# Optimization experiments

Hardware: AMD Instinct MI355X
Metric: run time of the kernel (lower is better)

## Reference

```python
import jax, jax.numpy as jnp
import numpy as np

H = 2048      # hidden_dim
DI = 4096     # intermediate_size
N = 128       # state_size
NH = 64       # num_heads
P = 64        # head_dim
K = 4         # conv kernel
CH = 256      # chunk size
L = 4096      # seq len
DT_MIN, DT_MAX = 1e-3, 1e2


def setup_inputs() -> dict:
    key = jax.random.key(0)
    ks = jax.random.split(key, 8)
    conv_dim = DI + 2 * N
    x = jax.random.normal(ks[0], (L, H), jnp.float32)
    W_in = jax.random.normal(ks[1], (DI + 2 * N + NH, H), jnp.float32) / np.sqrt(H)
    conv_w = jax.random.normal(ks[2], (conv_dim, 1, K), jnp.float32) / np.sqrt(K)
    conv_b = jax.random.normal(ks[3], (conv_dim,), jnp.float32) * 0.01
    u = jax.random.uniform(ks[4], (NH,))
    dt = jnp.exp(u * (np.log(0.1) - np.log(0.001)) + np.log(0.001))
    dt = jnp.maximum(dt, 1e-4)
    dt_bias = dt + jnp.log(-jnp.expm1(-dt))   # inverse-softplus init
    A_log = jnp.log(jax.random.uniform(ks[5], (NH,), minval=1.0, maxval=16.0))
    D = jnp.ones((NH,), jnp.float32)
    norm_w = jnp.ones((DI,), jnp.float32)
    W_out = jax.random.normal(ks[6], (H, DI), jnp.float32) / np.sqrt(DI)
    return dict(x=x, W_in=W_in, conv_w=conv_w, conv_b=conv_b, dt_bias=dt_bias,
                A_log=A_log, D=D, norm_w=norm_w, W_out=W_out)


def _causal_decay(a):
    # a: [..., T] per-step log-decays -> exp(segment sum) as lower-tri [..., T, T]
    T = a.shape[-1]
    strict = jnp.tril(jnp.ones((T, T), bool), -1)
    full = jnp.tril(jnp.ones((T, T), bool), 0)
    s = jnp.cumsum(jnp.where(strict, a[..., None], 0.0), axis=-2)
    return jnp.where(full, jnp.exp(s), 0.0)


def reference(x, W_in, conv_w, conv_b, dt_bias, A_log, D, norm_w, W_out):
    conv_dim = DI + 2 * N
    xBCdt = x @ W_in.T                                  # [L, DI+2N+NH]
    xBC, dt = xBCdt[:, :conv_dim], xBCdt[:, conv_dim:]
    # causal depthwise conv1d + SiLU
    z = jax.lax.conv_general_dilated(
        xBC.T[None], conv_w, (1,), [(K - 1, 0)],
        dimension_numbers=('NCH', 'OIH', 'NCH'),
        feature_group_count=conv_dim)[0] + conv_b[:, None]
    xBC = jax.nn.silu(z.T)                              # [L, conv_dim]
    x_ssm = xBC[:, :DI].reshape(L, NH, P)
    Bm = xBC[:, DI:DI + N]                              # [L, N] shared over heads
    Cm = xBC[:, DI + N:]                                # [L, N]
    dt = jnp.clip(jax.nn.softplus(dt + dt_bias), DT_MIN, DT_MAX)  # [L, NH]
    A = -jnp.exp(A_log.astype(jnp.float32))             # [NH]
    dA = dt * A                                         # [L, NH]
    xdt = x_ssm * dt[:, :, None]                        # [L, NH, P]
    nc = L // CH
    xc = xdt.reshape(nc, CH, NH, P)
    Bc = Bm.reshape(nc, CH, N)
    Cc = Cm.reshape(nc, CH, N)
    dAc = dA.reshape(nc, CH, NH)
    A_cs = jnp.cumsum(dAc, axis=1)                      # [c, k, h]
    # intra-chunk (diagonal blocks)
    Lmat = _causal_decay(dAc.transpose(0, 2, 1))        # [c, h, k, k]
    Y_diag = jnp.einsum('ckn,csn,chks,cshp->ckhp', Cc, Bc, Lmat, xc)
    # per-chunk right states
    decay_states = jnp.exp(A_cs[:, -1:, :] - A_cs)      # [c, k, h]
    states = jnp.einsum('ckn,ckh,ckhp->chpn', Bc, decay_states, xc)
    # inter-chunk recurrence (no initial state)
    chunk_sum = A_cs[:, -1, :].T                        # [h, c]
    dec = _causal_decay(jnp.pad(chunk_sum, ((0, 0), (1, 0))))  # [h, c+1, c+1]
    states = jnp.concatenate([jnp.zeros((1, NH, P, N), states.dtype), states], 0)
    new_states = jnp.einsum('hzc,chpn->zhpn', dec, states)      # [c+1, h, p, n]
    prev = new_states[:-1]                              # [c, h, p, n]
    Y_off = jnp.einsum('ckn,chpn,ckh->ckhp', Cc, prev, jnp.exp(A_cs))
    Y = (Y_diag + Y_off).reshape(L, NH, P) + x_ssm * D[None, :, None]
    y = Y.reshape(L, DI)
    # RMSNorm
    var = jnp.mean(jnp.square(y.astype(jnp.float32)), -1, keepdims=True)
    y = (y * jax.lax.rsqrt(var + 1e-6)) * norm_w
    return y @ W_out.T
```

## Files before the change

### kernel.cpp

```cpp
#include <hip/hip_runtime.h>


typedef __bf16 bf16;
typedef __bf16 bf16x8 __attribute__((ext_vector_type(8)));
typedef __bf16 bf16x4 __attribute__((ext_vector_type(4)));
typedef float  f32x4  __attribute__((ext_vector_type(4)));

#define DEV static __device__ __forceinline__

DEV f32x4 mfma16(bf16x8 a, bf16x8 b, f32x4 c) {
  return __builtin_amdgcn_mfma_f32_16x16x32_bf16(a, b, c, 0, 0, 0);
}

DEV void gll16(const bf16* g, bf16* l) {
  __builtin_amdgcn_global_load_lds(
      (const __attribute__((address_space(1))) unsigned int*)g,
      (__attribute__((address_space(3))) unsigned int*)l, 16, 0, 0);
}

#define BAR()   asm volatile("s_barrier" ::: "memory")
#define VMW(n)  asm volatile("s_waitcnt vmcnt(" #n ")" ::: "memory")

template <int NT, int LD, bool DTC>
__global__ __launch_bounds__(512, 4) void gemm_kernel(
    const bf16* __restrict__ Abase, const bf16* __restrict__ Bbase,
    bf16* __restrict__ C0, bf16* __restrict__ C1, float* __restrict__ dtf,
    int ldc, int ntN) {
  __shared__ __align__(16) bf16 lds[3 * 12288];
  const int tid = threadIdx.x;
  const int wid = tid >> 6, lane = tid & 63;
  const int lrow = lane & 15;
  const int lc = lane >> 4;
  const int wm = wid & 3, wn = wid >> 2;
  const int bx = blockIdx.x / ntN, by = blockIdx.x % ntN;
  const int row0 = bx * 256, col0 = by * 128;
  const bf16* A = Abase + (size_t)blockIdx.y * (NT * 32);
  const bf16* B = Bbase + (size_t)blockIdx.y * (NT * 32);

  const bf16* gA[2];
  const bf16* gB0;
#pragma unroll
  for (int q = 0; q < 2; ++q) {
    int P = q * 8192 + tid * 16;
    int Lq = P ^ (((P >> 7) & 3) << 4);
    int srow = Lq >> 6;
    int selem = (Lq & 63) >> 1;
    gA[q] = A + (size_t)(row0 + srow) * LD + selem;
  }
  {
    int P = tid * 16;
    int Lq = P ^ (((P >> 7) & 3) << 4);
    int srow = Lq >> 6;
    int selem = (Lq & 63) >> 1;
    gB0 = B + (size_t)(col0 + srow) * LD + selem;
  }
  auto stage = [&](int s, int ko) {
    bf16* sl = lds + s * 12288;
    gll16(gA[0] + ko, sl + tid * 8);
    gll16(gA[1] + ko, sl + 4096 + tid * 8);
    gll16(gB0 + ko, sl + 8192 + tid * 8);
  };
  auto rdA = [&](int s, int m) -> bf16x8 {
    int row = wm * 64 + m * 16 + lrow;
    int off = row * 64 + ((lc ^ ((row >> 1) & 3)) << 4);
    return *(const bf16x8*)((const char*)lds + s * 24576 + off);
  };
  auto rdB = [&](int s, int n) -> bf16x8 {
    int row = wn * 64 + n * 16 + lrow;
    int off = row * 64 + ((lc ^ ((row >> 1) & 3)) << 4);
    return *(const bf16x8*)((const char*)lds + s * 24576 + 16384 + off);
  };

  f32x4 acc[4][4] = {};
  stage(0, 0);
  stage(1, 32);
  int rs = 0, ws = 2;
  for (int t = 0; t < NT; ++t) {
    if (t + 1 < NT) { VMW(3); } else { VMW(0); }
    BAR();
    if (t + 2 < NT) stage(ws, (t + 2) * 32);
    bf16x8 b0 = rdB(rs, 0), b1 = rdB(rs, 1), b2 = rdB(rs, 2), b3 = rdB(rs, 3);
#pragma unroll
    for (int m = 0; m < 4; ++m) {
      bf16x8 a = rdA(rs, m);
      acc[m][0] = mfma16(a, b0, acc[m][0]);
      acc[m][1] = mfma16(a, b1, acc[m][1]);
      acc[m][2] = mfma16(a, b2, acc[m][2]);
      acc[m][3] = mfma16(a, b3, acc[m][3]);
    }
    rs = (rs == 2) ? 0 : rs + 1;
    ws = (ws == 2) ? 0 : ws + 1;
  }
  bf16* C = blockIdx.y ? C1 : C0;
  const int orow = lc * 4;
#pragma unroll
  for (int m = 0; m < 4; ++m)
#pragma unroll
    for (int n = 0; n < 4; ++n)
#pragma unroll
      for (int i = 0; i < 4; ++i) {
        int r = row0 + wm * 64 + m * 16 + orow + i;
        int c = col0 + wn * 64 + n * 16 + lrow;
        C[(size_t)r * ldc + c] = (bf16)acc[m][n][i];
      }
  if (DTC && by == 34 && wn == 0) {
#pragma unroll
    for (int m = 0; m < 4; ++m)
#pragma unroll
      for (int n = 0; n < 4; ++n)
#pragma unroll
        for (int i = 0; i < 4; ++i) {
          int r = row0 + wm * 64 + m * 16 + orow + i;
          int h = n * 16 + lrow;
          dtf[(size_t)r * 64 + h] = acc[m][n][i];
        }
  }
}

__global__ __launch_bounds__(256) void add2b_kernel(
    const bf16* __restrict__ a, const bf16* __restrict__ b,
    float* __restrict__ o, long n8) {
  long i = (long)blockIdx.x * blockDim.x + threadIdx.x;
  long stride = (long)gridDim.x * blockDim.x;
  for (; i < n8; i += stride) {
    bf16x8 va = ((const bf16x8*)a)[i];
    bf16x8 vb = ((const bf16x8*)b)[i];
    float4 o0, o1;
    o0.x = (float)va[0] + (float)vb[0];
    o0.y = (float)va[1] + (float)vb[1];
    o0.z = (float)va[2] + (float)vb[2];
    o0.w = (float)va[3] + (float)vb[3];
    o1.x = (float)va[4] + (float)vb[4];
    o1.y = (float)va[5] + (float)vb[5];
    o1.z = (float)va[6] + (float)vb[6];
    o1.w = (float)va[7] + (float)vb[7];
    ((float4*)o)[i * 2] = o0;
    ((float4*)o)[i * 2 + 1] = o1;
  }
}

__global__ __launch_bounds__(256) void cast_all_kernel(
    const float* __restrict__ x, bf16* __restrict__ xb,
    const float* __restrict__ W_in, bf16* __restrict__ winb,
    const float* __restrict__ W_out, bf16* __restrict__ woutb) {
  const long stride = (long)gridDim.x * blockDim.x;
  const long base = (long)blockIdx.x * blockDim.x + threadIdx.x;
  const long nx = (long)4096 * 2048 / 4;
  for (long i = base; i < nx; i += stride) {
    float4 v = ((const float4*)x)[i];
    ((bf16x4*)xb)[i] = bf16x4{(bf16)v.x, (bf16)v.y, (bf16)v.z, (bf16)v.w};
  }
  const long nw = (long)4608 * 2048 / 4;
  const long nwv = (long)4416 * 2048 / 4;
  for (long i = base; i < nw; i += stride) {
    bf16x4 o = {(bf16)0.f, (bf16)0.f, (bf16)0.f, (bf16)0.f};
    if (i < nwv) {
      float4 v = ((const float4*)W_in)[i];
      o = bf16x4{(bf16)v.x, (bf16)v.y, (bf16)v.z, (bf16)v.w};
    }
    ((bf16x4*)winb)[i] = o;
  }
  const long no = (long)2048 * 4096 / 4;
  for (long i = base; i < no; i += stride) {
    float4 v = ((const float4*)W_out)[i];
    ((bf16x4*)woutb)[i] = bf16x4{(bf16)v.x, (bf16)v.y, (bf16)v.z, (bf16)v.w};
  }
}

__global__ __launch_bounds__(256) void dt_scan_kernel(
    const float* __restrict__ dtf, const float* __restrict__ dt_bias,
    const float* __restrict__ A_log, float* __restrict__ dt,
    float* __restrict__ Acs, float* __restrict__ decayO,
    float* __restrict__ expAcs, float* __restrict__ csum) {
  const int c = blockIdx.x, h = blockIdx.y;
  const int k = threadIdx.x;
  const int t = c * 256 + k;
  __shared__ float buf[256];
  float raw = dtf[(size_t)t * 64 + h] + dt_bias[h];
  float dtv = raw > 20.f ? raw : log1pf(__expf(raw));
  dtv = fminf(fmaxf(dtv, 0.001f), 100.f);
  dt[(size_t)t * 64 + h] = dtv;
  float dA = -__expf(A_log[h]) * dtv;
  buf[k] = dA;
  __syncthreads();
  for (int off = 1; off < 256; off <<= 1) {
    float add = (k >= off) ? buf[k - off] : 0.f;
    __syncthreads();
    buf[k] += add;
    __syncthreads();
  }
  float v = buf[k];
  float total = buf[255];
  size_t base = (size_t)(c * 64 + h) * 256 + k;
  Acs[base] = v;
  expAcs[base] = __expf(v);
  decayO[base] = __expf(total - v);
  if (k == 0) csum[c * 64 + h] = total;
}

__global__ __launch_bounds__(256) void conv_kernel(
    const bf16* __restrict__ xbc, const float* __restrict__ conv_w,
    const float* __restrict__ conv_b, const float* __restrict__ dt,
    bf16* __restrict__ XS, bf16* __restrict__ XDT_T, bf16* __restrict__ Bm,
    bf16* __restrict__ BT, bf16* __restrict__ Cm) {
  const int t0 = blockIdx.x * 64;
  const int c0 = blockIdx.y * 64;
  __shared__ float lin[67 * 64];
  __shared__ bf16 tr[64 * 72];
  const int tid = threadIdx.x;
  for (int v = tid; v < 67 * 16; v += 256) {
    int r = v >> 4, c4 = (v & 15) * 4;
    int gt = t0 + r - 3;
    float4 f = {0.f, 0.f, 0.f, 0.f};
    if (gt >= 0) {
      bf16x4 b = *(const bf16x4*)(xbc + (size_t)gt * 4608 + c0 + c4);
      f.x = (float)b[0]; f.y = (float)b[1]; f.z = (float)b[2]; f.w = (float)b[3];
    }
    lin[r * 64 + c4 + 0] = f.x;
    lin[r * 64 + c4 + 1] = f.y;
    lin[r * 64 + c4 + 2] = f.z;
    lin[r * 64 + c4 + 3] = f.w;
  }
  __syncthreads();
  const int cl = tid & 63, tg = tid >> 6;
  const int ch = c0 + cl;
  const float w0 = conv_w[ch * 4 + 0], w1 = conv_w[ch * 4 + 1];
  const float w2 = conv_w[ch * 4 + 2], w3 = conv_w[ch * 4 + 3];
  const float bb = conv_b[ch];
  float vals[16];
  for (int j = 0; j < 16; ++j) {
    int tl = tg * 16 + j;
    float s = bb + lin[tl * 64 + cl] * w0 + lin[(tl + 1) * 64 + cl] * w1 +
              lin[(tl + 2) * 64 + cl] * w2 + lin[(tl + 3) * 64 + cl] * w3;
    vals[j] = s / (1.f + __expf(-s));
  }
  if (c0 < 4096) {
    const int hh = c0 >> 6;
    for (int j = 0; j < 16; ++j) {
      int t = t0 + tg * 16 + j;
      XS[(size_t)t * 4096 + ch] = (bf16)vals[j];
    }
    __syncthreads();
    for (int j = 0; j < 16; ++j) {
      int tl = tg * 16 + j;
      float dtv = dt[(size_t)(t0 + tl) * 64 + hh];
      tr[cl * 72 + tl] = (bf16)(vals[j] * dtv);
    }
    __syncthreads();
    int p = tid >> 2, toff = (tid & 3) * 16;
    bf16* dst = XDT_T + (size_t)(hh * 64 + p) * 4096 + t0 + toff;
    *(bf16x8*)(dst) = *(const bf16x8*)(tr + p * 72 + toff);
    *(bf16x8*)(dst + 8) = *(const bf16x8*)(tr + p * 72 + toff + 8);
  } else if (c0 < 4224) {
    const int n0 = c0 - 4096;
    for (int j = 0; j < 16; ++j) {
      int t = t0 + tg * 16 + j;
      Bm[(size_t)t * 128 + n0 + cl] = (bf16)vals[j];
    }
    __syncthreads();
    for (int j = 0; j < 16; ++j) tr[cl * 72 + tg * 16 + j] = (bf16)vals[j];
    __syncthreads();
    int p = tid >> 2, toff = (tid & 3) * 16;
    bf16* dst = BT + (size_t)(n0 + p) * 4096 + t0 + toff;
    *(bf16x8*)(dst) = *(const bf16x8*)(tr + p * 72 + toff);
    *(bf16x8*)(dst + 8) = *(const bf16x8*)(tr + p * 72 + toff + 8);
  } else {
    const int n0 = c0 - 4224;
    for (int j = 0; j < 16; ++j) {
      int t = t0 + tg * 16 + j;
      Cm[(size_t)t * 128 + n0 + cl] = (bf16)vals[j];
    }
  }
}

__global__ __launch_bounds__(256) void gmat_kernel(
    const bf16* __restrict__ Cm, const bf16* __restrict__ Bm,
    bf16* __restrict__ G) {
  const int c = blockIdx.x, kt = blockIdx.y, st = blockIdx.z;
  const int tid = threadIdx.x;
  const int wave = tid >> 6, lane = tid & 63;
  const int lrow = lane & 15, lk = (lane >> 4) * 8;
  const int wr = (wave >> 1) * 64, wc = (wave & 1) * 64;
  f32x4 acc[4][4] = {};
  for (int kk = 0; kk < 4; ++kk) {
    bf16x8 aF[4], bF[4];
    for (int m = 0; m < 4; ++m)
      aF[m] = *(const bf16x8*)(Cm + (size_t)(c * 256 + kt * 128 + wr + m * 16 + lrow) * 128 + kk * 32 + lk);
    for (int n = 0; n < 4; ++n)
      bF[n] = *(const bf16x8*)(Bm + (size_t)(c * 256 + st * 128 + wc + n * 16 + lrow) * 128 + kk * 32 + lk);
    for (int m = 0; m < 4; ++m)
      for (int n = 0; n < 4; ++n)
        acc[m][n] = mfma16(aF[m], bF[n], acc[m][n]);
  }
  const int orow = (lane >> 4) * 4;
  for (int m = 0; m < 4; ++m)
    for (int n = 0; n < 4; ++n)
      for (int i = 0; i < 4; ++i) {
        int k = kt * 128 + wr + m * 16 + orow + i;
        int s = st * 128 + wc + n * 16 + lrow;
        G[((size_t)c * 256 + k) * 256 + s] = (bf16)acc[m][n][i];
      }
}

__global__ __launch_bounds__(256) void states_kernel(
    const bf16* __restrict__ XDT_T, const bf16* __restrict__ BT,
    const float* __restrict__ decayO, bf16* __restrict__ states) {
  const int c = blockIdx.x, h = blockIdx.y;
  __shared__ bf16 Ap[64 * 264];
  __shared__ float sDec[256];
  const int tid = threadIdx.x;
  const int wave = tid >> 6, lane = tid & 63;
  const int lrow = lane & 15, lk = (lane >> 4) * 8;
  sDec[tid] = decayO[(size_t)(c * 64 + h) * 256 + tid];
  __syncthreads();
  {
    int p = tid >> 2, kb = (tid & 3) * 64;
    const bf16* src = XDT_T + (size_t)(h * 64 + p) * 4096 + c * 256 + kb;
    for (int j = 0; j < 8; ++j) {
      bf16x8 v = *(const bf16x8*)(src + j * 8);
      bf16x8 o;
      for (int i = 0; i < 8; ++i) o[i] = (bf16)((float)v[i] * sDec[kb + j * 8 + i]);
      *(bf16x8*)(Ap + p * 264 + kb + j * 8) = o;
    }
  }
  __syncthreads();
  const int nb = wave * 32;
  f32x4 acc[4][2] = {};
  for (int kk = 0; kk < 8; ++kk) {
    bf16x8 aF[4], bF[2];
    for (int m = 0; m < 4; ++m)
      aF[m] = *(const bf16x8*)(Ap + (m * 16 + lrow) * 264 + kk * 32 + lk);
    for (int n = 0; n < 2; ++n)
      bF[n] = *(const bf16x8*)(BT + (size_t)(nb + n * 16 + lrow) * 4096 + c * 256 + kk * 32 + lk);
    for (int m = 0; m < 4; ++m)
      for (int n = 0; n < 2; ++n)
        acc[m][n] = mfma16(aF[m], bF[n], acc[m][n]);
  }
  bf16* st = states + (size_t)(c * 64 + h) * 64 * 128;
  const int orow = (lane >> 4) * 4;
  for (int m = 0; m < 4; ++m)
    for (int n = 0; n < 2; ++n)
      for (int i = 0; i < 4; ++i)
        st[(size_t)(m * 16 + orow + i) * 128 + nb + n * 16 + lrow] = (bf16)acc[m][n][i];
}

__global__ __launch_bounds__(128) void chunk_rec_kernel(
    const bf16* __restrict__ states, const float* __restrict__ csum,
    bf16* __restrict__ prev) {
  const int h = blockIdx.x, p = blockIdx.y;
  const int n = threadIdx.x;
  size_t base = (size_t)h * 64 * 128 + (size_t)p * 128 + n;
  float run = 0.f;
  for (int c = 0; c < 16; ++c) {
    size_t idx = (size_t)c * 64 * 64 * 128 + base;
    prev[idx] = (bf16)run;
    run = run * __expf(csum[c * 64 + h]) + (float)states[idx];
  }
}

__global__ __launch_bounds__(256) void ydiag_kernel(
    const bf16* __restrict__ Cm, const bf16* __restrict__ prev,
    const bf16* __restrict__ Gb, const float* __restrict__ Acs,
    const float* __restrict__ expAcs, const bf16* __restrict__ XDT_T,
    bf16* __restrict__ Yb) {
  const int c = blockIdx.x, h = blockIdx.y;
  __shared__ float sAcs[256];
  __shared__ float sExp[256];
  __shared__ __align__(16) bf16 pv[64 * 136];
  __shared__ __align__(16) bf16 xd[64 * 264];
  const int tid = threadIdx.x;
  const int wave = tid >> 6, lane = tid & 63;
  const int lrow = lane & 15, lk = (lane >> 4) * 8;
  const int wv16 = wave * 16;
  sAcs[tid] = Acs[(size_t)(c * 64 + h) * 256 + tid];
  sExp[tid] = expAcs[(size_t)(c * 64 + h) * 256 + tid];
  {
    int r = tid >> 2, q = (tid & 3) * 32;
    const bf16* src = prev + (size_t)(c * 64 + h) * 8192 + r * 128 + q;
    bf16* dst = pv + r * 136 + q;
    for (int j = 0; j < 4; ++j)
      *(bf16x8*)(dst + j * 8) = *(const bf16x8*)(src + j * 8);
  }
  {
    int r = tid >> 2, q = (tid & 3) * 64;
    const bf16* src = XDT_T + (size_t)(h * 64 + r) * 4096 + c * 256 + q;
    bf16* dst = xd + r * 264 + q;
    for (int j = 0; j < 8; ++j)
      *(bf16x8*)(dst + j * 8) = *(const bf16x8*)(src + j * 8);
  }
  __syncthreads();
  f32x4 acc[4][4] = {};
  bf16x8 aYo[4][4];
#pragma unroll
  for (int kk = 0; kk < 4; ++kk)
#pragma unroll
    for (int m = 0; m < 4; ++m)
      aYo[kk][m] = *(const bf16x8*)(Cm + (size_t)(c * 256 + m * 64 + wv16 + lrow) * 128 + kk * 32 + lk);
#pragma unroll
  for (int kk = 0; kk < 4; ++kk) {
    bf16x8 bF[4];
#pragma unroll
    for (int n = 0; n < 4; ++n)
      bF[n] = *(const bf16x8*)(pv + (n * 16 + lrow) * 136 + kk * 32 + lk);
#pragma unroll
    for (int m = 0; m < 4; ++m)
#pragma unroll
      for (int n = 0; n < 4; ++n)
        acc[m][n] = mfma16(aYo[kk][m], bF[n], acc[m][n]);
  }
  const int orow = (lane >> 4) * 4;
#pragma unroll
  for (int m = 0; m < 4; ++m)
#pragma unroll
    for (int i = 0; i < 4; ++i) {
      float e = sExp[m * 64 + wv16 + orow + i];
      for (int n = 0; n < 4; ++n) acc[m][n][i] *= e;
    }
  const bf16* Gp = Gb + (size_t)c * 65536;
#pragma unroll
  for (int stile = 0; stile < 4; ++stile) {
    const int s0 = stile * 64;
    bf16x8 graw[2][4];
#pragma unroll
    for (int kk = 0; kk < 2; ++kk)
#pragma unroll
      for (int m = 0; m < 4; ++m)
        if (m * 64 + wv16 + 15 >= s0) {
          int row = m * 64 + wv16 + lrow;
          graw[kk][m] = *(const bf16x8*)(Gp + (size_t)row * 256 + s0 + kk * 32 + lk);
        }
    bf16x8 bF[2][4];
#pragma unroll
    for (int kk = 0; kk < 2; ++kk)
#pragma unroll
      for (int n = 0; n < 4; ++n)
        bF[kk][n] = *(const bf16x8*)(xd + (n * 16 + lrow) * 264 + s0 + kk * 32 + lk);
#pragma unroll
    for (int kk = 0; kk < 2; ++kk)
#pragma unroll
      for (int m = 0; m < 4; ++m) {
        if (m * 64 + wv16 + 15 < s0) continue;
        const int row = m * 64 + wv16 + lrow;
        const float ak = sAcs[row];
        bf16x8 af;
#pragma unroll
        for (int j = 0; j < 8; ++j) {
          int s = s0 + kk * 32 + lk + j;
          float v = (float)graw[kk][m][j] * __expf(ak - sAcs[s]);
          if (s > row) v = 0.f;
          af[j] = (bf16)v;
        }
#pragma unroll
        for (int n = 0; n < 4; ++n)
          acc[m][n] = mfma16(af, bF[kk][n], acc[m][n]);
      }
  }
#pragma unroll
  for (int m = 0; m < 4; ++m)
#pragma unroll
    for (int n = 0; n < 4; ++n)
#pragma unroll
      for (int i = 0; i < 4; ++i) {
        int t = c * 256 + m * 64 + wv16 + orow + i;
        int col = h * 64 + n * 16 + lrow;
        Yb[(size_t)t * 4096 + col] = (bf16)acc[m][n][i];
      }
}

__global__ __launch_bounds__(256) void rmsnorm_kernel(
    const bf16* __restrict__ Yb, const bf16* __restrict__ XS,
    const float* __restrict__ Dp, const float* __restrict__ norm_w,
    bf16* __restrict__ out) {
  const int row = blockIdx.x;
  const bf16x4* y4 = (const bf16x4*)(Yb + (size_t)row * 4096);
  const bf16x4* xs4 = (const bf16x4*)(XS + (size_t)row * 4096);
  float4 v[4];
  float ss = 0.f;
  for (int j = 0; j < 4; ++j) {
    int c4 = threadIdx.x + j * 256;
    bf16x4 yb = y4[c4];
    bf16x4 xs = xs4[c4];
    float d = Dp[(c4 * 4) >> 6];
    float4 y;
    y.x = (float)yb[0] + (float)xs[0] * d;
    y.y = (float)yb[1] + (float)xs[1] * d;
    y.z = (float)yb[2] + (float)xs[2] * d;
    y.w = (float)yb[3] + (float)xs[3] * d;
    v[j] = y;
    ss += y.x * y.x + y.y * y.y + y.z * y.z + y.w * y.w;
  }
  for (int off = 32; off; off >>= 1) ss += __shfl_down(ss, off, 64);
  __shared__ float ws[4];
  if ((threadIdx.x & 63) == 0) ws[threadIdx.x >> 6] = ss;
  __syncthreads();
  float scale = rsqrtf((ws[0] + ws[1] + ws[2] + ws[3]) / 4096.f + 1e-6f);
  for (int j = 0; j < 4; ++j) {
    int col = (threadIdx.x + j * 256) * 4;
    float4 w = *(const float4*)(norm_w + col);
    bf16x4 o = {(bf16)(v[j].x * scale * w.x), (bf16)(v[j].y * scale * w.y),
                (bf16)(v[j].z * scale * w.z), (bf16)(v[j].w * scale * w.w)};
    *(bf16x4*)(out + (size_t)row * 4096 + col) = o;
  }
}

extern "C" void kernel_launch(void* const* d_in, const int* in_sizes, int n_in,
                              void* d_out, int out_size, void* d_ws, size_t ws_size,
                              hipStream_t stream) {
  const float* x       = (const float*)d_in[0];
  const float* W_in    = (const float*)d_in[1];
  const float* conv_w  = (const float*)d_in[2];
  const float* conv_b  = (const float*)d_in[3];
  const float* dt_bias = (const float*)d_in[4];
  const float* A_log   = (const float*)d_in[5];
  const float* Dp      = (const float*)d_in[6];
  const float* norm_w  = (const float*)d_in[7];
  const float* W_out   = (const float*)d_in[8];

  size_t o = 0;
  char* base = (char*)d_ws;
  auto take = [&](size_t b) {
    char* p = base + o;
    o += (b + 255) & ~(size_t)255;
    return (void*)p;
  };
  bf16*  xb     = (bf16*)take((size_t)4096 * 2048 * 2);
  bf16*  winb   = (bf16*)take((size_t)4608 * 2048 * 2);
  bf16*  xbc    = (bf16*)take((size_t)4096 * 4608 * 2);
  float* dtf    = (float*)take((size_t)4096 * 64 * 4);
  float* dtg    = (float*)take((size_t)4096 * 64 * 4);
  float* Acs    = (float*)take((size_t)4096 * 64 * 4);
  float* decayO = (float*)take((size_t)4096 * 64 * 4);
  float* expA   = (float*)take((size_t)4096 * 64 * 4);
  float* csum   = (float*)take((size_t)16 * 64 * 4);
  bf16*  XS     = (bf16*)take((size_t)4096 * 4096 * 2);
  bf16*  XDT_T  = (bf16*)take((size_t)4096 * 4096 * 2);
  bf16*  Bm     = (bf16*)take((size_t)4096 * 128 * 2);
  bf16*  BT     = (bf16*)take((size_t)4096 * 128 * 2);
  bf16*  Cm     = (bf16*)take((size_t)4096 * 128 * 2);
  bf16*  Yb     = (bf16*)take((size_t)4096 * 4096 * 2);
  bf16*  prev   = (bf16*)take((size_t)16 * 64 * 64 * 128 * 2);
  bf16*  woutb  = (bf16*)take((size_t)2048 * 4096 * 2);
  bf16*  Gb     = (bf16*)((char*)xbc);
  bf16*  states = (bf16*)((char*)xbc + (size_t)4194304);
  bf16*  ynorm  = xb;
  bf16*  p2a    = XS;
  bf16*  p2b    = XDT_T;

  cast_all_kernel<<<2048, 256, 0, stream>>>(x, xb, W_in, winb, W_out, woutb);
  gemm_kernel<64, 2048, true><<<dim3(576, 1), 512, 0, stream>>>(
      xb, winb, xbc, xbc, dtf, 4608, 36);
  dt_scan_kernel<<<dim3(16, 64), 256, 0, stream>>>(dtf, dt_bias, A_log, dtg,
                                                   Acs, decayO, expA, csum);
  conv_kernel<<<dim3(64, 68), 256, 0, stream>>>(xbc, conv_w, conv_b, dtg, XS,
                                                XDT_T, Bm, BT, Cm);
  gmat_kernel<<<dim3(16, 2, 2), 256, 0, stream>>>(Cm, Bm, Gb);
  states_kernel<<<dim3(16, 64), 256, 0, stream>>>(XDT_T, BT, decayO, states);
  chunk_rec_kernel<<<dim3(64, 64), 128, 0, stream>>>(states, csum, prev);
  ydiag_kernel<<<dim3(16, 64), 256, 0, stream>>>(Cm, prev, Gb, Acs, expA,
                                                 XDT_T, Yb);
  rmsnorm_kernel<<<4096, 256, 0, stream>>>(Yb, XS, Dp, norm_w, ynorm);
  gemm_kernel<64, 4096, false><<<dim3(256, 2), 512, 0, stream>>>(
      ynorm, woutb, p2a, p2b, nullptr, 2048, 16);
  add2b_kernel<<<2048, 256, 0, stream>>>(p2a, p2b, (float*)d_out,
                                         (long)4096 * 2048 / 8);
}
```

Baseline: 327.8 us.

## Rewrite GEMMs with 256x256 tiles, 8-phase ping-pong schedule, split-K input projection

Replaces the 256x128, BK=32 triple-buffered GEMM with a 256x256 tile, BK=64 double-buffered kernel. Each K step is split into four MFMA phases that interleave LDS reads and async global-to-LDS loads, using barriers, setprio and sched_barrier, with a new LDS swizzle. The input projection now uses 2-way split-K, writing two partial outputs that conv and dt_scan sum when they read them. The aim is more reuse per tile and better overlap of loads with math. In exchange it runs one block per CU with 128 fp32 accumulators per lane and adds extra memory traffic for the split-K partials.

```diff
diff --git a/kernel.cpp b/kernel.cpp
--- a/kernel.cpp
+++ b/kernel.cpp
@@ -19,100 +19,173 @@
 }
 
 #define BAR()   asm volatile("s_barrier" ::: "memory")
+#define LGKM0() do { asm volatile("s_waitcnt lgkmcnt(0)" ::: "memory"); \
+                     __builtin_amdgcn_sched_barrier(0); } while (0)
 #define VMW(n)  asm volatile("s_waitcnt vmcnt(" #n ")" ::: "memory")
+#define SCHB()  __builtin_amdgcn_sched_barrier(0)
 
 template <int NT, int LD, bool DTC>
-__global__ __launch_bounds__(512, 4) void gemm_kernel(
+__global__ __launch_bounds__(512, 1) void gemm8_kernel(
     const bf16* __restrict__ Abase, const bf16* __restrict__ Bbase,
-    bf16* __restrict__ C0, bf16* __restrict__ C1, float* __restrict__ dtf,
-    int ldc, int ntN) {
-  __shared__ __align__(16) bf16 lds[3 * 12288];
+    bf16* __restrict__ C0, bf16* __restrict__ C1,
+    float* __restrict__ dt0, float* __restrict__ dt1, int ldc, int ntN) {
+  __shared__ __align__(16) bf16 lds[2 * 32768];
   const int tid = threadIdx.x;
   const int wid = tid >> 6, lane = tid & 63;
   const int lrow = lane & 15;
   const int lc = lane >> 4;
-  const int wm = wid & 3, wn = wid >> 2;
+  const int wm = wid & 1, wn = wid >> 1;
   const int bx = blockIdx.x / ntN, by = blockIdx.x % ntN;
-  const int row0 = bx * 256, col0 = by * 128;
-  const bf16* A = Abase + (size_t)blockIdx.y * (NT * 32);
-  const bf16* B = Bbase + (size_t)blockIdx.y * (NT * 32);
-
-  const bf16* gA[2];
-  const bf16* gB0;
-#pragma unroll
-  for (int q = 0; q < 2; ++q) {
-    int P = q * 8192 + tid * 16;
-    int Lq = P ^ (((P >> 7) & 3) << 4);
-    int srow = Lq >> 6;
-    int selem = (Lq & 63) >> 1;
-    gA[q] = A + (size_t)(row0 + srow) * LD + selem;
-  }
-  {
-    int P = tid * 16;
-    int Lq = P ^ (((P >> 7) & 3) << 4);
-    int srow = Lq >> 6;
-    int selem = (Lq & 63) >> 1;
-    gB0 = B + (size_t)(col0 + srow) * LD + selem;
-  }
-  auto stage = [&](int s, int ko) {
-    bf16* sl = lds + s * 12288;
-    gll16(gA[0] + ko, sl + tid * 8);
-    gll16(gA[1] + ko, sl + 4096 + tid * 8);
-    gll16(gB0 + ko, sl + 8192 + tid * 8);
+  const int row0 = bx * 256, col0 = by * 256;
+  const bf16* A = Abase + (size_t)blockIdx.y * (NT * 64);
+  const bf16* B = Bbase + (size_t)blockIdx.y * (NT * 64);
+
+  const bf16* srcA[2][2];
+  const bf16* srcB[2][2];
+#pragma unroll
+  for (int h = 0; h < 2; ++h)
+#pragma unroll
+    for (int s = 0; s < 2; ++s) {
+      int P = h * 16384 + s * 8192 + tid * 16;
+      int rl = P >> 7;
+      int idx = rl & 127;
+      int Ra = ((idx >> 6) << 7) + h * 64 + (idx & 63);
+      int ca = (P & 127) ^ ((Ra & 7) << 4);
+      srcA[h][s] = A + (size_t)(row0 + Ra) * LD + (ca >> 1);
+      int Rb = ((idx >> 5) << 6) + h * 32 + (idx & 31);
+      int cb = (P & 127) ^ ((Rb & 7) << 4);
+      srcB[h][s] = B + (size_t)(col0 + Rb) * LD + (cb >> 1);
+    }
+  auto stA = [&](int b, int h, int ko) {
+    bf16* d = lds + b * 32768 + h * 8192 + tid * 8;
+    gll16(srcA[h][0] + ko, d);
+    gll16(srcA[h][1] + ko, d + 4096);
   };
-  auto rdA = [&](int s, int m) -> bf16x8 {
-    int row = wm * 64 + m * 16 + lrow;
-    int off = row * 64 + ((lc ^ ((row >> 1) & 3)) << 4);
-    return *(const bf16x8*)((const char*)lds + s * 24576 + off);
+  auto stB = [&](int b, int h, int ko) {
+    bf16* d = lds + b * 32768 + 16384 + h * 8192 + tid * 8;
+    gll16(srcB[h][0] + ko, d);
+    gll16(srcB[h][1] + ko, d + 4096);
   };
-  auto rdB = [&](int s, int n) -> bf16x8 {
-    int row = wn * 64 + n * 16 + lrow;
-    int off = row * 64 + ((lc ^ ((row >> 1) & 3)) << 4);
-    return *(const bf16x8*)((const char*)lds + s * 24576 + 16384 + off);
+  auto rdA = [&](int b, int row, int ks) -> bf16x8 {
+    int lin = (((row >> 6) & 1) << 7) + ((row >> 7) << 6) + (row & 63);
+    int cb = (ks * 64 + lc * 16) ^ ((row & 7) << 4);
+    return *(const bf16x8*)((const char*)lds + b * 65536 + lin * 128 + cb);
   };
-
-  f32x4 acc[4][4] = {};
-  stage(0, 0);
-  stage(1, 32);
-  int rs = 0, ws = 2;
+  auto rdB = [&](int b, int row, int ks) -> bf16x8 {
+    int lin = (((row >> 5) & 1) << 7) + ((row >> 6) << 5) + (row & 31);
+    int cb = (ks * 64 + lc * 16) ^ ((row & 7) << 4);
+    return *(const bf16x8*)((const char*)lds + b * 65536 + 32768 + lin * 128 + cb);
+  };
+
+  f32x4 acc[8][4] = {};
+  bf16x8 aF[4][2], bF[4][2];
+
+  stB(0, 0, 0); stB(0, 1, 0); stA(0, 0, 0); stA(0, 1, 0);
+  VMW(2);
+  BAR();
+
   for (int t = 0; t < NT; ++t) {
-    if (t + 1 < NT) { VMW(3); } else { VMW(0); }
+    const int bt = t & 1, bn = bt ^ 1;
+    const int ko = (t + 1) * 64;
+    const bool pf = (t + 1 < NT);
+#pragma unroll
+    for (int nf = 0; nf < 2; ++nf)
+#pragma unroll
+      for (int ks = 0; ks < 2; ++ks)
+        bF[nf][ks] = rdB(bt, wn * 64 + nf * 16 + lrow, ks);
+#pragma unroll
+    for (int mf = 0; mf < 4; ++mf)
+#pragma unroll
+      for (int ks = 0; ks < 2; ++ks)
+        aF[mf][ks] = rdA(bt, wm * 128 + mf * 16 + lrow, ks);
+    if (pf) stB(bn, 0, ko);
+    BAR(); LGKM0();
+    __builtin_amdgcn_s_setprio(1);
+#pragma unroll
+    for (int mf = 0; mf < 4; ++mf)
+#pragma unroll
+      for (int nf = 0; nf < 2; ++nf)
+#pragma unroll
+        for (int ks = 0; ks < 2; ++ks)
+          acc[mf][nf] = mfma16(aF[mf][ks], bF[nf][ks], acc[mf][nf]);
+    __builtin_amdgcn_s_setprio(0);
+    SCHB();
     BAR();
-    if (t + 2 < NT) stage(ws, (t + 2) * 32);
-    bf16x8 b0 = rdB(rs, 0), b1 = rdB(rs, 1), b2 = rdB(rs, 2), b3 = rdB(rs, 3);
-#pragma unroll
-    for (int m = 0; m < 4; ++m) {
-      bf16x8 a = rdA(rs, m);
-      acc[m][0] = mfma16(a, b0, acc[m][0]);
-      acc[m][1] = mfma16(a, b1, acc[m][1]);
-      acc[m][2] = mfma16(a, b2, acc[m][2]);
-      acc[m][3] = mfma16(a, b3, acc[m][3]);
-    }
-    rs = (rs == 2) ? 0 : rs + 1;
-    ws = (ws == 2) ? 0 : ws + 1;
+#pragma unroll
+    for (int nf = 2; nf < 4; ++nf)
+#pragma unroll
+      for (int ks = 0; ks < 2; ++ks)
+        bF[nf][ks] = rdB(bt, wn * 64 + nf * 16 + lrow, ks);
+    if (pf) stB(bn, 1, ko);
+    BAR(); LGKM0();
+    __builtin_amdgcn_s_setprio(1);
+#pragma unroll
+    for (int mf = 0; mf < 4; ++mf)
+#pragma unroll
+      for (int nf = 2; nf < 4; ++nf)
+#pragma unroll
+        for (int ks = 0; ks < 2; ++ks)
+          acc[mf][nf] = mfma16(aF[mf][ks], bF[nf][ks], acc[mf][nf]);
+    __builtin_amdgcn_s_setprio(0);
+    SCHB();
+    if (pf) { VMW(4); } else { VMW(0); }
+    BAR();
+#pragma unroll
+    for (int mf = 0; mf < 4; ++mf)
+#pragma unroll
+      for (int ks = 0; ks < 2; ++ks)
+        aF[mf][ks] = rdA(bt, wm * 128 + 64 + mf * 16 + lrow, ks);
+    if (pf) stA(bn, 0, ko);
+    BAR(); LGKM0();
+    __builtin_amdgcn_s_setprio(1);
+#pragma unroll
+    for (int mf = 0; mf < 4; ++mf)
+#pragma unroll
+      for (int nf = 2; nf < 4; ++nf)
+#pragma unroll
+        for (int ks = 0; ks < 2; ++ks)
+          acc[mf + 4][nf] = mfma16(aF[mf][ks], bF[nf][ks], acc[mf + 4][nf]);
+    __builtin_amdgcn_s_setprio(0);
+    SCHB();
+    BAR();
+    if (pf) stA(bn, 1, ko);
+    BAR();
+    __builtin_amdgcn_s_setprio(1);
+#pragma unroll
+    for (int mf = 0; mf < 4; ++mf)
+#pragma unroll
+      for (int nf = 0; nf < 2; ++nf)
+#pragma unroll
+        for (int ks = 0; ks < 2; ++ks)
+          acc[mf + 4][nf] = mfma16(aF[mf][ks], bF[nf][ks], acc[mf + 4][nf]);
+    __builtin_amdgcn_s_setprio(0);
+    SCHB();
+    if (pf) { VMW(2); }
+    BAR();
   }
   bf16* C = blockIdx.y ? C1 : C0;
   const int orow = lc * 4;
 #pragma unroll
-  for (int m = 0; m < 4; ++m)
-#pragma unroll
-    for (int n = 0; n < 4; ++n)
+  for (int mf = 0; mf < 8; ++mf)
+#pragma unroll
+    for (int nf = 0; nf < 4; ++nf)
 #pragma unroll
       for (int i = 0; i < 4; ++i) {
-        int r = row0 + wm * 64 + m * 16 + orow + i;
-        int c = col0 + wn * 64 + n * 16 + lrow;
-        C[(size_t)r * ldc + c] = (bf16)acc[m][n][i];
+        int r = row0 + wm * 128 + mf * 16 + orow + i;
+        int c = col0 + wn * 64 + nf * 16 + lrow;
+        C[(size_t)r * ldc + c] = (bf16)acc[mf][nf][i];
       }
-  if (DTC && by == 34 && wn == 0) {
-#pragma unroll
-    for (int m = 0; m < 4; ++m)
-#pragma unroll
-      for (int n = 0; n < 4; ++n)
+  if (DTC && by == 17 && wn == 0) {
+    float* dtp = blockIdx.y ? dt1 : dt0;
+#pragma unroll
+    for (int mf = 0; mf < 8; ++mf)
+#pragma unroll
+      for (int nf = 0; nf < 4; ++nf)
 #pragma unroll
         for (int i = 0; i < 4; ++i) {
-          int r = row0 + wm * 64 + m * 16 + orow + i;
-          int h = n * 16 + lrow;
-          dtf[(size_t)r * 64 + h] = acc[m][n][i];
+          int r = row0 + wm * 128 + mf * 16 + orow + i;
+          int h = nf * 16 + lrow;
+          dtp[(size_t)r * 64 + h] = acc[mf][nf][i];
         }
   }
 }
@@ -168,15 +241,16 @@
 }
 
 __global__ __launch_bounds__(256) void dt_scan_kernel(
-    const float* __restrict__ dtf, const float* __restrict__ dt_bias,
-    const float* __restrict__ A_log, float* __restrict__ dt,
-    float* __restrict__ Acs, float* __restrict__ decayO,
+    const float* __restrict__ dt0, const float* __restrict__ dt1,
+    const float* __restrict__ dt_bias, const float* __restrict__ A_log,
+    float* __restrict__ dt, float* __restrict__ Acs, float* __restrict__ decayO,
     float* __restrict__ expAcs, float* __restrict__ csum) {
   const int c = blockIdx.x, h = blockIdx.y;
   const int k = threadIdx.x;
   const int t = c * 256 + k;
   __shared__ float buf[256];
-  float raw = dtf[(size_t)t * 64 + h] + dt_bias[h];
+  size_t idx = (size_t)t * 64 + h;
+  float raw = dt0[idx] + dt1[idx] + dt_bias[h];
   float dtv = raw > 20.f ? raw : log1pf(__expf(raw));
   dtv = fminf(fmaxf(dtv, 0.001f), 100.f);
   dt[(size_t)t * 64 + h] = dtv;
@@ -199,10 +273,11 @@
 }
 
 __global__ __launch_bounds__(256) void conv_kernel(
-    const bf16* __restrict__ xbc, const float* __restrict__ conv_w,
-    const float* __restrict__ conv_b, const float* __restrict__ dt,
-    bf16* __restrict__ XS, bf16* __restrict__ XDT_T, bf16* __restrict__ Bm,
-    bf16* __restrict__ BT, bf16* __restrict__ Cm) {
+    const bf16* __restrict__ xp0, const bf16* __restrict__ xp1,
+    const float* __restrict__ conv_w, const float* __restrict__ conv_b,
+    const float* __restrict__ dt, bf16* __restrict__ XS,
+    bf16* __restrict__ XDT_T, bf16* __restrict__ Bm, bf16* __restrict__ BT,
+    bf16* __restrict__ Cm) {
   const int t0 = blockIdx.x * 64;
   const int c0 = blockIdx.y * 64;
   __shared__ float lin[67 * 64];
@@ -213,8 +288,13 @@
     int gt = t0 + r - 3;
     float4 f = {0.f, 0.f, 0.f, 0.f};
     if (gt >= 0) {
-      bf16x4 b = *(const bf16x4*)(xbc + (size_t)gt * 4608 + c0 + c4);
-      f.x = (float)b[0]; f.y = (float)b[1]; f.z = (float)b[2]; f.w = (float)b[3];
+      size_t g = (size_t)gt * 4608 + c0 + c4;
+      bf16x4 b0 = *(const bf16x4*)(xp0 + g);
+      bf16x4 b1 = *(const bf16x4*)(xp1 + g);
+      f.x = (float)b0[0] + (float)b1[0];
+      f.y = (float)b0[1] + (float)b1[1];
+      f.z = (float)b0[2] + (float)b1[2];
+      f.w = (float)b0[3] + (float)b1[3];
     }
     lin[r * 64 + c4 + 0] = f.x;
     lin[r * 64 + c4 + 1] = f.y;
@@ -525,8 +605,10 @@
   };
   bf16*  xb     = (bf16*)take((size_t)4096 * 2048 * 2);
   bf16*  winb   = (bf16*)take((size_t)4608 * 2048 * 2);
-  bf16*  xbc    = (bf16*)take((size_t)4096 * 4608 * 2);
-  float* dtf    = (float*)take((size_t)4096 * 64 * 4);
+  bf16*  xp0b   = (bf16*)take((size_t)4096 * 4608 * 2);
+  bf16*  xp1b   = (bf16*)take((size_t)4096 * 4608 * 2);
+  float* dt0    = (float*)take((size_t)4096 * 64 * 4);
+  float* dt1    = (float*)take((size_t)4096 * 64 * 4);
   float* dtg    = (float*)take((size_t)4096 * 64 * 4);
   float* Acs    = (float*)take((size_t)4096 * 64 * 4);
   float* decayO = (float*)take((size_t)4096 * 64 * 4);
@@ -540,27 +622,27 @@
   bf16*  Yb     = (bf16*)take((size_t)4096 * 4096 * 2);
   bf16*  prev   = (bf16*)take((size_t)16 * 64 * 64 * 128 * 2);
   bf16*  woutb  = (bf16*)take((size_t)2048 * 4096 * 2);
-  bf16*  Gb     = (bf16*)((char*)xbc);
-  bf16*  states = (bf16*)((char*)xbc + (size_t)4194304);
+  bf16*  Gb     = (bf16*)((char*)xp0b);
+  bf16*  states = (bf16*)((char*)xp0b + (size_t)4194304);
   bf16*  ynorm  = xb;
   bf16*  p2a    = XS;
   bf16*  p2b    = XDT_T;
 
   cast_all_kernel<<<2048, 256, 0, stream>>>(x, xb, W_in, winb, W_out, woutb);
-  gemm_kernel<64, 2048, true><<<dim3(576, 1), 512, 0, stream>>>(
-      xb, winb, xbc, xbc, dtf, 4608, 36);
-  dt_scan_kernel<<<dim3(16, 64), 256, 0, stream>>>(dtf, dt_bias, A_log, dtg,
-                                                   Acs, decayO, expA, csum);
-  conv_kernel<<<dim3(64, 68), 256, 0, stream>>>(xbc, conv_w, conv_b, dtg, XS,
-                                                XDT_T, Bm, BT, Cm);
+  gemm8_kernel<16, 2048, true><<<dim3(288, 2), 512, 0, stream>>>(
+      xb, winb, xp0b, xp1b, dt0, dt1, 4608, 18);
+  dt_scan_kernel<<<dim3(16, 64), 256, 0, stream>>>(dt0, dt1, dt_bias, A_log,
+                                                   dtg, Acs, decayO, expA, csum);
+  conv_kernel<<<dim3(64, 68), 256, 0, stream>>>(xp0b, xp1b, conv_w, conv_b,
+                                                dtg, XS, XDT_T, Bm, BT, Cm);
   gmat_kernel<<<dim3(16, 2, 2), 256, 0, stream>>>(Cm, Bm, Gb);
   states_kernel<<<dim3(16, 64), 256, 0, stream>>>(XDT_T, BT, decayO, states);
   chunk_rec_kernel<<<dim3(64, 64), 128, 0, stream>>>(states, csum, prev);
   ydiag_kernel<<<dim3(16, 64), 256, 0, stream>>>(Cm, prev, Gb, Acs, expA,
                                                  XDT_T, Yb);
   rmsnorm_kernel<<<4096, 256, 0, stream>>>(Yb, XS, Dp, norm_w, ynorm);
-  gemm_kernel<64, 4096, false><<<dim3(256, 2), 512, 0, stream>>>(
-      ynorm, woutb, p2a, p2b, nullptr, 2048, 16);
+  gemm8_kernel<32, 4096, false><<<dim3(128, 2), 512, 0, stream>>>(
+      ynorm, woutb, p2a, p2b, nullptr, nullptr, 2048, 8);
   add2b_kernel<<<2048, 256, 0, stream>>>(p2a, p2b, (float*)d_out,
                                          (long)4096 * 2048 / 8);
 }
```

New measurement: 326.0 us. Within noise of the previous version (-0.5%).

## Shrink GEMM tile to 128x128 with four waves and double buffering

Applied to the files above, without the earlier changes.

The shared GEMM kernel moves from a 256x128 block tile with 8 waves and a 3-stage LDS pipeline to a 128x128 tile with 4 waves and 2 LDS buffers. A unified loader issues four 16-byte global-to-LDS loads per thread for A and B. Each iteration ends with a full vmcnt(0) wait and a barrier. Grids double to keep coverage. The aim is more blocks per CU and less LDS per block, at the cost of lower operand reuse per block and less latency hiding from the shallower pipeline.

```diff
diff --git a/kernel.cpp b/kernel.cpp
--- a/kernel.cpp
+++ b/kernel.cpp
@@ -22,74 +22,67 @@
 #define VMW(n)  asm volatile("s_waitcnt vmcnt(" #n ")" ::: "memory")
 
 template <int NT, int LD, bool DTC>
-__global__ __launch_bounds__(512, 4) void gemm_kernel(
+__global__ __launch_bounds__(256, 4) void gemm_kernel(
     const bf16* __restrict__ Abase, const bf16* __restrict__ Bbase,
     bf16* __restrict__ C0, bf16* __restrict__ C1, float* __restrict__ dtf,
     int ldc, int ntN) {
-  __shared__ __align__(16) bf16 lds[3 * 12288];
+  __shared__ __align__(16) bf16 lds[2 * 8192];
   const int tid = threadIdx.x;
   const int wid = tid >> 6, lane = tid & 63;
   const int lrow = lane & 15;
   const int lc = lane >> 4;
-  const int wm = wid & 3, wn = wid >> 2;
+  const int wm = wid & 1, wn = wid >> 1;
   const int bx = blockIdx.x / ntN, by = blockIdx.x % ntN;
-  const int row0 = bx * 256, col0 = by * 128;
+  const int row0 = bx * 128, col0 = by * 128;
   const bf16* A = Abase + (size_t)blockIdx.y * (NT * 32);
   const bf16* B = Bbase + (size_t)blockIdx.y * (NT * 32);
 
-  const bf16* gA[2];
-  const bf16* gB0;
-#pragma unroll
-  for (int q = 0; q < 2; ++q) {
-    int P = q * 8192 + tid * 16;
-    int Lq = P ^ (((P >> 7) & 3) << 4);
-    int srow = Lq >> 6;
-    int selem = (Lq & 63) >> 1;
-    gA[q] = A + (size_t)(row0 + srow) * LD + selem;
-  }
-  {
-    int P = tid * 16;
-    int Lq = P ^ (((P >> 7) & 3) << 4);
-    int srow = Lq >> 6;
-    int selem = (Lq & 63) >> 1;
-    gB0 = B + (size_t)(col0 + srow) * LD + selem;
+  const bf16* gsrc[4];
+#pragma unroll
+  for (int q = 0; q < 4; ++q) {
+    int P = q * 4096 + tid * 16;
+    int r = P >> 6;
+    int rloc = r & 127;
+    int c = (P & 63) ^ (((rloc >> 1) & 3) << 4);
+    gsrc[q] = (r < 128) ? A + (size_t)(row0 + rloc) * LD + (c >> 1)
+                        : B + (size_t)(col0 + rloc) * LD + (c >> 1);
   }
   auto stage = [&](int s, int ko) {
-    bf16* sl = lds + s * 12288;
-    gll16(gA[0] + ko, sl + tid * 8);
-    gll16(gA[1] + ko, sl + 4096 + tid * 8);
-    gll16(gB0 + ko, sl + 8192 + tid * 8);
+    bf16* sl = lds + s * 8192;
+#pragma unroll
+    for (int q = 0; q < 4; ++q) gll16(gsrc[q] + ko, sl + q * 2048 + tid * 8);
   };
   auto rdA = [&](int s, int m) -> bf16x8 {
     int row = wm * 64 + m * 16 + lrow;
     int off = row * 64 + ((lc ^ ((row >> 1) & 3)) << 4);
-    return *(const bf16x8*)((const char*)lds + s * 24576 + off);
+    return *(const bf16x8*)((const char*)lds + s * 16384 + off);
   };
   auto rdB = [&](int s, int n) -> bf16x8 {
     int row = wn * 64 + n * 16 + lrow;
     int off = row * 64 + ((lc ^ ((row >> 1) & 3)) << 4);
-    return *(const bf16x8*)((const char*)lds + s * 24576 + 16384 + off);
+    return *(const bf16x8*)((const char*)lds + s * 16384 + 8192 + off);
   };
 
   f32x4 acc[4][4] = {};
   stage(0, 0);
-  stage(1, 32);
-  int rs = 0, ws = 2;
+  VMW(0);
+  BAR();
   for (int t = 0; t < NT; ++t) {
-    if (t + 1 < NT) { VMW(3); } else { VMW(0); }
-    BAR();
-    if (t + 2 < NT) stage(ws, (t + 2) * 32);
-    bf16x8 b0 = rdB(rs, 0), b1 = rdB(rs, 1), b2 = rdB(rs, 2), b3 = rdB(rs, 3);
+    const int s = t & 1;
+    if (t + 1 < NT) stage(s ^ 1, (t + 1) * 32);
+    bf16x8 b0 = rdB(s, 0), b1 = rdB(s, 1), b2 = rdB(s, 2), b3 = rdB(s, 3);
 #pragma unroll
     for (int m = 0; m < 4; ++m) {
-      bf16x8 a = rdA(rs, m);
+      bf16x8 a = rdA(s, m);
       acc[m][0] = mfma16(a, b0, acc[m][0]);
       acc[m][1] = mfma16(a, b1, acc[m][1]);
       acc[m][2] = mfma16(a, b2, acc[m][2]);
       acc[m][3] = mfma16(a, b3, acc[m][3]);
     }
-    rs = (rs == 2) ? 0 : rs + 1;
-    ws = (ws == 2) ? 0 : ws + 1;
+    if (t + 1 < NT) {
+      VMW(0);
+      BAR();
+    }
   }
   bf16* C = blockIdx.y ? C1 : C0;
   const int orow = lc * 4;
@@ -547,7 +540,7 @@
   bf16*  p2b    = XDT_T;
 
   cast_all_kernel<<<2048, 256, 0, stream>>>(x, xb, W_in, winb, W_out, woutb);
-  gemm_kernel<64, 2048, true><<<dim3(576, 1), 512, 0, stream>>>(
+  gemm_kernel<64, 2048, true><<<dim3(1152, 1), 256, 0, stream>>>(
       xb, winb, xbc, xbc, dtf, 4608, 36);
   dt_scan_kernel<<<dim3(16, 64), 256, 0, stream>>>(dtf, dt_bias, A_log, dtg,
                                                    Acs, decayO, expA, csum);
@@ -559,7 +552,7 @@
   ydiag_kernel<<<dim3(16, 64), 256, 0, stream>>>(Cm, prev, Gb, Acs, expA,
                                                  XDT_T, Yb);
   rmsnorm_kernel<<<4096, 256, 0, stream>>>(Yb, XS, Dp, norm_w, ynorm);
-  gemm_kernel<64, 4096, false><<<dim3(256, 2), 512, 0, stream>>>(
+  gemm_kernel<64, 4096, false><<<dim3(512, 2), 256, 0, stream>>>(
       ynorm, woutb, p2a, p2b, nullptr, 2048, 16);
   add2b_kernel<<<2048, 256, 0, stream>>>(p2a, p2b, (float*)d_out,
                                          (long)4096 * 2048 / 8);
```

Result: slower. 338.9 us (+3.4%).

## Replace split-K output GEMM plus add kernel with single full-K 128x128 GEMM

Applied to the files above, without the earlier changes.

The output projection used to split K into two halves across blockIdx.y, write two bf16 partial products, and then sum them in a separate add kernel into fp32. It is replaced by a new 256-thread GEMM with 128x128 tiles that runs the full K=4096 loop and writes fp32 output directly. This removes the extra kernel launch, the intermediate bf16 round-trip through memory, and the precision loss from rounding the partials. In exchange there is less K-parallelism per tile, and the smaller tiles give lower arithmetic intensity.

```diff
diff --git a/kernel.cpp b/kernel.cpp
--- a/kernel.cpp
+++ b/kernel.cpp
@@ -24,8 +24,7 @@
 template <int NT, int LD, bool DTC>
 __global__ __launch_bounds__(512, 4) void gemm_kernel(
     const bf16* __restrict__ Abase, const bf16* __restrict__ Bbase,
-    bf16* __restrict__ C0, bf16* __restrict__ C1, float* __restrict__ dtf,
-    int ldc, int ntN) {
+    bf16* __restrict__ C0, float* __restrict__ dtf, int ldc, int ntN) {
   __shared__ __align__(16) bf16 lds[3 * 12288];
   const int tid = threadIdx.x;
   const int wid = tid >> 6, lane = tid & 63;
@@ -34,8 +33,8 @@
   const int wm = wid & 3, wn = wid >> 2;
   const int bx = blockIdx.x / ntN, by = blockIdx.x % ntN;
   const int row0 = bx * 256, col0 = by * 128;
-  const bf16* A = Abase + (size_t)blockIdx.y * (NT * 32);
-  const bf16* B = Bbase + (size_t)blockIdx.y * (NT * 32);
+  const bf16* A = Abase;
+  const bf16* B = Bbase;
 
   const bf16* gA[2];
   const bf16* gB0;
@@ -91,7 +90,6 @@
     rs = (rs == 2) ? 0 : rs + 1;
     ws = (ws == 2) ? 0 : ws + 1;
   }
-  bf16* C = blockIdx.y ? C1 : C0;
   const int orow = lc * 4;
 #pragma unroll
   for (int m = 0; m < 4; ++m)
@@ -101,7 +99,7 @@
       for (int i = 0; i < 4; ++i) {
         int r = row0 + wm * 64 + m * 16 + orow + i;
         int c = col0 + wn * 64 + n * 16 + lrow;
-        C[(size_t)r * ldc + c] = (bf16)acc[m][n][i];
+        C0[(size_t)r * ldc + c] = (bf16)acc[m][n][i];
       }
   if (DTC && by == 34 && wn == 0) {
 #pragma unroll
@@ -117,26 +115,76 @@
   }
 }
 
-__global__ __launch_bounds__(256) void add2b_kernel(
-    const bf16* __restrict__ a, const bf16* __restrict__ b,
-    float* __restrict__ o, long n8) {
-  long i = (long)blockIdx.x * blockDim.x + threadIdx.x;
-  long stride = (long)gridDim.x * blockDim.x;
-  for (; i < n8; i += stride) {
-    bf16x8 va = ((const bf16x8*)a)[i];
-    bf16x8 vb = ((const bf16x8*)b)[i];
-    float4 o0, o1;
-    o0.x = (float)va[0] + (float)vb[0];
-    o0.y = (float)va[1] + (float)vb[1];
-    o0.z = (float)va[2] + (float)vb[2];
-    o0.w = (float)va[3] + (float)vb[3];
-    o1.x = (float)va[4] + (float)vb[4];
-    o1.y = (float)va[5] + (float)vb[5];
-    o1.z = (float)va[6] + (float)vb[6];
-    o1.w = (float)va[7] + (float)vb[7];
-    ((float4*)o)[i * 2] = o0;
-    ((float4*)o)[i * 2 + 1] = o1;
-  }
+template <int NT, int LD>
+__global__ __launch_bounds__(256, 3) void gemm2_kernel(
+    const bf16* __restrict__ Abase, const bf16* __restrict__ Bbase,
+    float* __restrict__ C, int ldc, int ntN) {
+  __shared__ __align__(16) bf16 lds[3 * 8192];
+  const int tid = threadIdx.x;
+  const int wid = tid >> 6, lane = tid & 63;
+  const int lrow = lane & 15;
+  const int lc = lane >> 4;
+  const int wm = wid & 1, wn = wid >> 1;
+  const int bx = blockIdx.x / ntN, by = blockIdx.x % ntN;
+  const int row0 = bx * 128, col0 = by * 128;
+
+  const bf16* gsrc[4];
+#pragma unroll
+  for (int q = 0; q < 4; ++q) {
+    int P = q * 4096 + tid * 16;
+    int r = P >> 6;
+    int rloc = r & 127;
+    int c = (P & 63) ^ (((rloc >> 1) & 3) << 4);
+    gsrc[q] = (r < 128) ? Abase + (size_t)(row0 + rloc) * LD + (c >> 1)
+                        : Bbase + (size_t)(col0 + rloc) * LD + (c >> 1);
+  }
+  auto stage = [&](int s, int ko) {
+    bf16* sl = lds + s * 8192;
+#pragma unroll
+    for (int q = 0; q < 4; ++q) gll16(gsrc[q] + ko, sl + q * 2048 + tid * 8);
+  };
+  auto rdA = [&](int s, int m) -> bf16x8 {
+    int row = wm * 64 + m * 16 + lrow;
+    int off = row * 64 + ((lc ^ ((row >> 1) & 3)) << 4);
+    return *(const bf16x8*)((const char*)lds + s * 16384 + off);
+  };
+  auto rdB = [&](int s, int n) -> bf16x8 {
+    int row = wn * 64 + n * 16 + lrow;
+    int off = row * 64 + ((lc ^ ((row >> 1) & 3)) << 4);
+    return *(const bf16x8*)((const char*)lds + s * 16384 + 8192 + off);
+  };
+
+  f32x4 acc[4][4] = {};
+  stage(0, 0);
+  stage(1, 32);
+  int rs = 0, ws = 2;
+  for (int t = 0; t < NT; ++t) {
+    if (t + 1 < NT) { VMW(4); } else { VMW(0); }
+    BAR();
+    if (t + 2 < NT) stage(ws, (t + 2) * 32);
+    bf16x8 b0 = rdB(rs, 0), b1 = rdB(rs, 1), b2 = rdB(rs, 2), b3 = rdB(rs, 3);
+#pragma unroll
+    for (int m = 0; m < 4; ++m) {
+      bf16x8 a = rdA(rs, m);
+      acc[m][0] = mfma16(a, b0, acc[m][0]);
+      acc[m][1] = mfma16(a, b1, acc[m][1]);
+      acc[m][2] = mfma16(a, b2, acc[m][2]);
+      acc[m][3] = mfma16(a, b3, acc[m][3]);
+    }
+    rs = (rs == 2) ? 0 : rs + 1;
+    ws = (ws == 2) ? 0 : ws + 1;
+  }
+  const int orow = lc * 4;
+#pragma unroll
+  for (int m = 0; m < 4; ++m)
+#pragma unroll
+    for (int n = 0; n < 4; ++n)
+#pragma unroll
+      for (int i = 0; i < 4; ++i) {
+        int r = row0 + wm * 64 + m * 16 + orow + i;
+        int c = col0 + wn * 64 + n * 16 + lrow;
+        C[(size_t)r * ldc + c] = acc[m][n][i];
+      }
 }
 
 __global__ __launch_bounds__(256) void cast_all_kernel(
@@ -543,12 +591,10 @@
   bf16*  Gb     = (bf16*)((char*)xbc);
   bf16*  states = (bf16*)((char*)xbc + (size_t)4194304);
   bf16*  ynorm  = xb;
-  bf16*  p2a    = XS;
-  bf16*  p2b    = XDT_T;
 
   cast_all_kernel<<<2048, 256, 0, stream>>>(x, xb, W_in, winb, W_out, woutb);
   gemm_kernel<64, 2048, true><<<dim3(576, 1), 512, 0, stream>>>(
-      xb, winb, xbc, xbc, dtf, 4608, 36);
+      xb, winb, xbc, dtf, 4608, 36);
   dt_scan_kernel<<<dim3(16, 64), 256, 0, stream>>>(dtf, dt_bias, A_log, dtg,
                                                    Acs, decayO, expA, csum);
   conv_kernel<<<dim3(64, 68), 256, 0, stream>>>(xbc, conv_w, conv_b, dtg, XS,
@@ -559,8 +605,6 @@
   ydiag_kernel<<<dim3(16, 64), 256, 0, stream>>>(Cm, prev, Gb, Acs, expA,
                                                  XDT_T, Yb);
   rmsnorm_kernel<<<4096, 256, 0, stream>>>(Yb, XS, Dp, norm_w, ynorm);
-  gemm_kernel<64, 4096, false><<<dim3(256, 2), 512, 0, stream>>>(
-      ynorm, woutb, p2a, p2b, nullptr, 2048, 16);
-  add2b_kernel<<<2048, 256, 0, stream>>>(p2a, p2b, (float*)d_out,
-                                         (long)4096 * 2048 / 8);
-}
+  gemm2_kernel<128, 4096><<<dim3(512, 1), 256, 0, stream>>>(
+      ynorm, woutb, (float*)d_out, 2048, 16);
+}
```

New measurement: 323.2 us. About the same (-1.4%).
